# Kernel optimization log

Measured on AMD Instinct MI355X. Metric: run time of the kernel, lower is better.

## Reference

```python
import jax, jax.numpy as jnp
from jax import lax
import numpy as np

B, W, D = 32, 256, 512      # batch, input_window, d_model == feature_size
NHID = W // 2               # GAT hidden per head = 128
NHEADS = 4
ALPHA = 0.1                 # LeakyReLU slope (GAT default)
NEG = -1e9                  # masked-softmax fill


def conv1d(x, w, b):
    # x: [B, C, L], w: [O, I, K=3], 'same' padding, stride 1
    y = lax.conv_general_dilated(x, w, (1,), 'SAME', dimension_numbers=('NCH', 'OIH', 'NCH'))
    return y + b[None, :, None]


def gat_heads(h, adj, Wt, bb, ai, ai_b, aj, aj_b):
    # h: [B, N, F_in], adj: [B, N, N]; vectorized over NHEADS heads
    Wh = jnp.einsum('bnf,hof->bhno', h, Wt) + bb[None, :, None, :]   # [B,H,N,NHID]
    e1 = jnp.einsum('bhno,ho->bhn', Wh, ai) + ai_b[None, :, None]
    e2 = jnp.einsum('bhno,ho->bhn', Wh, aj) + aj_b[None, :, None]
    e = jax.nn.leaky_relu(e1[..., :, None] + e2[..., None, :], ALPHA)  # [B,H,N,N]
    att = jax.nn.softmax(jnp.where(adj[:, None] > 0, e, NEG), axis=-1)
    return jnp.einsum('bhnm,bhmo->bhno', att, Wh)


def gat_out(h, adj, Wt, bb, ai, ai_b, aj, aj_b):
    # h: [B, N, NHEADS*NHID] -> [B, N, W]
    Wh = h @ Wt.T + bb
    e1 = Wh @ ai + ai_b
    e2 = Wh @ aj + aj_b
    e = jax.nn.leaky_relu(e1[:, :, None] + e2[:, None, :], ALPHA)
    att = jax.nn.softmax(jnp.where(adj > 0, e, NEG), axis=-1)
    return jnp.einsum('bnm,bmo->bno', att, Wh)


def setup_inputs() -> dict:
    key = jax.random.key(0)
    ks = jax.random.split(key, 16)
    f32 = jnp.float32
    def xu(k, shape, fan_in):
        return jax.random.normal(k, shape, f32) * (1.414 / np.sqrt(fan_in))
    return {
        'x': jax.random.normal(ks[0], (B, W, D), f32),
        'qW': xu(ks[1], (D, D, 3), 3 * D), 'qb': jnp.zeros((D,), f32),
        'kW': xu(ks[2], (D, D, 3), 3 * D), 'kb': jnp.zeros((D,), f32),
        'vW': xu(ks[3], (D, D, 3), 3 * D), 'vb': jnp.zeros((D,), f32),
        'head_W': xu(ks[4], (NHEADS, NHID, W), W), 'head_b': jnp.zeros((NHEADS, NHID), f32),
        'head_ai': xu(ks[5], (NHEADS, NHID), NHID), 'head_ai_b': jnp.zeros((NHEADS,), f32),
        'head_aj': xu(ks[6], (NHEADS, NHID), NHID), 'head_aj_b': jnp.zeros((NHEADS,), f32),
        'out_W': xu(ks[7], (W, NHEADS * NHID), NHEADS * NHID), 'out_b': jnp.zeros((W,), f32),
        'out_ai': xu(ks[8], (W,), W), 'out_ai_b': jnp.zeros((), f32),
        'out_aj': xu(ks[9], (W,), W), 'out_aj_b': jnp.zeros((), f32),
        'proj_W': xu(ks[10], (D, D), D), 'proj_b': jnp.zeros((D,), f32),
    }


def reference(x, qW, qb, kW, kb, vW, vb,
              head_W, head_b, head_ai, head_ai_b, head_aj, head_aj_b,
              out_W, out_b, out_ai, out_ai_b, out_aj, out_aj_b,
              proj_W, proj_b):
    b, w, f = x.shape
    xt = jnp.transpose(x, (0, 2, 1))                 # [B, D, W]
    q = conv1d(xt, qW, qb)
    k = conv1d(xt, kW, kb)
    v = conv1d(xt, vW, vb)
    scale = 1.0 / jnp.sqrt(jnp.asarray(f, x.dtype))  # q.shape[-2] == d_model
    adj = jax.nn.sigmoid(jnp.einsum('bdw,bew->bde', q, k) * scale)  # [B, D, D]
    # GAT: nodes = feature dims (N=D), node features = window (W); dropout skipped (eval)
    hh = jax.nn.elu(gat_heads(v, adj, head_W, head_b, head_ai, head_ai_b, head_aj, head_aj_b))
    hcat = jnp.transpose(hh, (0, 2, 1, 3)).reshape(b, f, NHEADS * NHID)  # [B, D, 4*NHID]
    g = gat_out(hcat, adj, out_W, out_b, out_ai, out_ai_b, out_aj, out_aj_b)
    gat_y = jax.nn.log_softmax(jax.nn.elu(g), axis=2)  # [B, D, W]
    out = jnp.transpose(gat_y, (0, 2, 1)) @ proj_W.T + proj_b  # [B, W, D]
    return (out, adj)
```

## Files before the change

kernel.cpp:

```cpp
#include <hip/hip_runtime.h>
#include <math.h>

typedef unsigned short u16;
typedef __attribute__((ext_vector_type(8))) short short8;
typedef __attribute__((ext_vector_type(4))) float f32x4;

#define BB 32
#define WW 256
#define DD 512
#define NHEADS 4
#define NHID 128

__device__ __forceinline__ u16 f2bf(float f) {
  union { float f; unsigned int i; } x; x.f = f;
  unsigned int i = x.i;
  i += 0x7fffu + ((i >> 16) & 1u);
  return (u16)(i >> 16);
}
__device__ __forceinline__ float bf2f(u16 u) {
  union { float f; unsigned int i; } x; x.i = ((unsigned int)u) << 16; return x.f;
}

union BF8 { short8 v; u16 u[8]; };
union BF4 { ushort4 v; u16 u[4]; };

__global__ __launch_bounds__(256) void kprep_w(
    const float* __restrict__ qW, const float* __restrict__ kW, const float* __restrict__ vW,
    u16* __restrict__ Wt)
{
  int idx = blockIdx.x*256 + threadIdx.x;
  if (idx >= 3*DD*DD) return;
  int c = idx >> 18;
  int oi = idx & (DD*DD - 1);
  int i = oi & (DD-1);
  int o = oi >> 9;
  const float* W = (c==0) ? qW : (c==1) ? kW : vW;
  float w0 = W[oi*3+0], w1 = W[oi*3+1], w2 = W[oi*3+2];
  Wt[((size_t)(c*3+0)*DD + o)*DD + i] = f2bf(w0);
  Wt[((size_t)(c*3+1)*DD + o)*DD + i] = f2bf(w1);
  Wt[((size_t)(c*3+2)*DD + o)*DD + i] = f2bf(w2);
}

__global__ __launch_bounds__(256) void kcvt(const float* __restrict__ s, u16* __restrict__ d, int n) {
  int i = blockIdx.x*256 + threadIdx.x;
  if (i < n) d[i] = f2bf(s[i]);
}

__global__ __launch_bounds__(256) void kprep_a(
    const float* __restrict__ hW, const float* __restrict__ hai, const float* __restrict__ haib,
    const float* __restrict__ haj, const float* __restrict__ hajb,
    const float* __restrict__ hb,
    const float* __restrict__ oW, const float* __restrict__ oai, const float* __restrict__ oaib,
    const float* __restrict__ oaj, const float* __restrict__ oajb,
    const float* __restrict__ ob,
    float* __restrict__ ahat_i, float* __restrict__ ahat_j,
    float* __restrict__ oahat_i, float* __restrict__ oahat_j,
    float* __restrict__ cvec)
{
  int idx = blockIdx.x*256 + threadIdx.x;
  if (idx < 1024) {
    int h = idx >> 8, f = idx & 255;
    float s = 0.f;
    for (int o = 0; o < NHID; ++o) s += hW[((size_t)h*NHID + o)*WW + f] * hai[h*NHID + o];
    ahat_i[idx] = s;
  } else if (idx < 2048) {
    int t = idx - 1024; int h = t >> 8, f = t & 255;
    float s = 0.f;
    for (int o = 0; o < NHID; ++o) s += hW[((size_t)h*NHID + o)*WW + f] * haj[h*NHID + o];
    ahat_j[t] = s;
  } else if (idx < 2560) {
    int f = idx - 2048;
    float s = 0.f;
    for (int o = 0; o < WW; ++o) s += oW[(size_t)o*DD + f] * oai[o];
    oahat_i[f] = s;
  } else if (idx < 3072) {
    int f = idx - 2560;
    float s = 0.f;
    for (int o = 0; o < WW; ++o) s += oW[(size_t)o*DD + f] * oaj[o];
    oahat_j[f] = s;
  } else if (idx < 3082) {
    int t = idx - 3072;
    if (t < 4) {
      float s = 0.f;
      for (int o = 0; o < NHID; ++o) s += hb[t*NHID + o]*hai[t*NHID + o];
      cvec[t] = s + haib[t];
    } else if (t < 8) {
      int h = t - 4; float s = 0.f;
      for (int o = 0; o < NHID; ++o) s += hb[h*NHID + o]*haj[h*NHID + o];
      cvec[t] = s + hajb[h];
    } else if (t == 8) {
      float s = 0.f;
      for (int o = 0; o < WW; ++o) s += ob[o]*oai[o];
      cvec[8] = s + oaib[0];
    } else {
      float s = 0.f;
      for (int o = 0; o < WW; ++o) s += ob[o]*oaj[o];
      cvec[9] = s + oajb[0];
    }
  }
}

__global__ __launch_bounds__(256) void kprep_x(
    const float* __restrict__ x, int zb, int nrow8, u16* __restrict__ xpad)
{
  int idx8 = blockIdx.x*256 + threadIdx.x;
  if (idx8 >= nrow8) return;
  int i8 = idx8 & 63;
  int rowg = idx8 >> 6;
  int z = rowg / 258, r = rowg - z*258;
  int t = r - 1;
  BF8 o8;
  if (t >= 0 && t < WW) {
    const float* src = x + ((size_t)(zb+z)*WW + t)*DD + i8*8;
    float4 v0 = *reinterpret_cast<const float4*>(src);
    float4 v1 = *reinterpret_cast<const float4*>(src + 4);
    o8.u[0]=f2bf(v0.x); o8.u[1]=f2bf(v0.y); o8.u[2]=f2bf(v0.z); o8.u[3]=f2bf(v0.w);
    o8.u[4]=f2bf(v1.x); o8.u[5]=f2bf(v1.y); o8.u[6]=f2bf(v1.z); o8.u[7]=f2bf(v1.w);
  } else {
    #pragma unroll
    for (int j = 0; j < 8; ++j) o8.u[j] = 0;
  }
  *reinterpret_cast<short8*>(xpad + (size_t)rowg*DD + i8*8) = o8.v;
}

__global__ __launch_bounds__(256) void k1_mfma(
    const u16* __restrict__ xpad, const u16* __restrict__ Wt,
    const float* __restrict__ qb, const float* __restrict__ kb, const float* __restrict__ vb,
    u16* __restrict__ qbf, u16* __restrict__ kbf, u16* __restrict__ vbf)
{
  __shared__ u16 bt[2][130*64];
  const int tid = threadIdx.x;
  const int w  = tid >> 6;
  const int l  = tid & 63;
  const int ln = l & 15;
  const int kg = l >> 4;
  const int og = blockIdx.x * 64 + w * 16;
  const int t0 = blockIdx.y * 128;
  const int z  = blockIdx.z;

  const u16* A0 = Wt + (size_t)(og + ln)*DD + kg*8;
  const u16* Xb = xpad + ((size_t)z*258 + t0)*DD;

  f32x4 acc[3][8];
  #pragma unroll
  for (int c=0;c<3;++c)
    #pragma unroll
    for (int ts=0;ts<8;++ts) acc[c][ts] = (f32x4){0.f,0.f,0.f,0.f};

  short8 ArP[9], ArQ[9];
  short8 sg0, sg1, sg2, sg3, sg4;
  const int ccw = tid & 7;
  const int rs = tid >> 3;

#define K1_LOADX(i0v) do { \
    sg0 = *reinterpret_cast<const short8*>(Xb + (size_t)rs*DD + (i0v) + ccw*8); \
    sg1 = *reinterpret_cast<const short8*>(Xb + (size_t)(rs+32)*DD + (i0v) + ccw*8); \
    sg2 = *reinterpret_cast<const short8*>(Xb + (size_t)(rs+64)*DD + (i0v) + ccw*8); \
    sg3 = *reinterpret_cast<const short8*>(Xb + (size_t)(rs+96)*DD + (i0v) + ccw*8); \
    if (tid < 16) sg4 = *reinterpret_cast<const short8*>(Xb + (size_t)(rs+128)*DD + (i0v) + ccw*8); \
  } while(0)

#define K1_WRITEX(bufv) do { \
    *reinterpret_cast<short8*>(&bt[bufv][rs*64 + ((ccw^(rs&7))<<3)]) = sg0; \
    *reinterpret_cast<short8*>(&bt[bufv][(rs+32)*64 + ((ccw^((rs+32)&7))<<3)]) = sg1; \
    *reinterpret_cast<short8*>(&bt[bufv][(rs+64)*64 + ((ccw^((rs+64)&7))<<3)]) = sg2; \
    *reinterpret_cast<short8*>(&bt[bufv][(rs+96)*64 + ((ccw^((rs+96)&7))<<3)]) = sg3; \
    if (tid < 16) *reinterpret_cast<short8*>(&bt[bufv][(rs+128)*64 + ((ccw^((rs+128)&7))<<3)]) = sg4; \
  } while(0)

#define K1_LOADA(Abuf, i0v, khv) do { \
    _Pragma("unroll") \
    for (int c = 0; c < 3; ++c) { \
      _Pragma("unroll") \
      for (int tap = 0; tap < 3; ++tap) \
        Abuf[c*3+tap] = *reinterpret_cast<const short8*>(A0 + (size_t)(c*3+tap)*DD*DD + (i0v) + (khv)*32); \
    } \
  } while(0)

#define K1_MFMAS(Abuf, khv) do { \
    _Pragma("unroll") \
    for (int tap = 0; tap < 3; ++tap) { \
      _Pragma("unroll") \
      for (int ts = 0; ts < 8; ++ts) { \
        int row = ts*16 + ln + tap; \
        short8 bfr = *reinterpret_cast<const short8*>(&bt[cur][row*64 + ((((khv)*4+kg) ^ (row&7))<<3)]); \
        acc[0][ts] = __builtin_amdgcn_mfma_f32_16x16x32_bf16(Abuf[0*3+tap], bfr, acc[0][ts], 0,0,0); \
        acc[1][ts] = __builtin_amdgcn_mfma_f32_16x16x32_bf16(Abuf[1*3+tap], bfr, acc[1][ts], 0,0,0); \
        acc[2][ts] = __builtin_amdgcn_mfma_f32_16x16x32_bf16(Abuf[2*3+tap], bfr, acc[2][ts], 0,0,0); \
      } \
    } \
  } while(0)

  K1_LOADX(0);
  K1_LOADA(ArP, 0, 0);
  K1_WRITEX(0);
  __syncthreads();

  int cur = 0;
  #pragma unroll 1
  for (int p = 0; p < 8; ++p) {
    const int i0 = p*64;
    if (p < 7) K1_LOADX(i0 + 64);
    K1_LOADA(ArQ, i0, 1);
    K1_MFMAS(ArP, 0);
    const int i0n = (p < 7) ? i0 + 64 : 0;
    K1_LOADA(ArP, i0n, 0);
    K1_MFMAS(ArQ, 1);
    if (p < 7) {
      K1_WRITEX(cur ^ 1);
      __syncthreads();
      cur ^= 1;
    }
  }

#undef K1_LOADX
#undef K1_WRITEX
#undef K1_LOADA
#undef K1_MFMAS

  #pragma unroll
  for (int ts=0; ts<8; ++ts) {
    int tg = t0 + ts*16 + ln;
    #pragma unroll
    for (int r=0;r<4;++r) {
      int o = og + kg*4 + r;
      size_t oi = (size_t)(z*DD + o)*WW + tg;
      qbf[oi] = f2bf(acc[0][ts][r] + qb[o]);
      kbf[oi] = f2bf(acc[1][ts][r] + kb[o]);
      vbf[oi] = f2bf(acc[2][ts][r] + vb[o]);
    }
  }
}


__global__ __launch_bounds__(256) void k2_adj(
    const u16* __restrict__ qbf, const u16* __restrict__ kbf, int zb, float* __restrict__ adjo)
{
  __shared__ u16 bp[2][64*64];
  const int tid = threadIdx.x;
  const int w = tid >> 6, l = tid & 63, ln = l & 15, kg = l >> 4;
  const int d0 = blockIdx.x*64 + w*16;
  const int e0 = blockIdx.y*64;
  const int z  = blockIdx.z;
  const int sc = tid & 7, sr = tid >> 3;
  const int sp = sc ^ (sr & 7);
  const int sp2 = sc ^ ((sr+32) & 7);
  const u16* B0 = kbf + (size_t)(z*DD + e0)*WW;
  const u16* Asrc = qbf + (size_t)(z*DD + d0 + ln)*WW + kg*8;

  f32x4 acc[4];
  #pragma unroll
  for (int es=0;es<4;++es) acc[es] = (f32x4){0.f,0.f,0.f,0.f};
  short8 aP0, aP1, aQ0, aQ1, sg0, sg1;

  sg0 = *reinterpret_cast<const short8*>(B0 + (size_t)sr*WW + sc*8);
  sg1 = *reinterpret_cast<const short8*>(B0 + (size_t)(sr+32)*WW + sc*8);
  aP0 = *reinterpret_cast<const short8*>(Asrc);
  aP1 = *reinterpret_cast<const short8*>(Asrc + 32);
  *reinterpret_cast<short8*>(&bp[0][sr*64 + sp*8]) = sg0;
  *reinterpret_cast<short8*>(&bp[0][(sr+32)*64 + sp2*8]) = sg1;
  __syncthreads();

  int cur = 0;
  #pragma unroll 1
  for (int s = 0; s < 4; ++s) {
    const int fn = (s+1)*64;
    if (s < 3) {
      sg0 = *reinterpret_cast<const short8*>(B0 + (size_t)sr*WW + fn + sc*8);
      sg1 = *reinterpret_cast<const short8*>(B0 + (size_t)(sr+32)*WW + fn + sc*8);
      aQ0 = *reinterpret_cast<const short8*>(Asrc + fn);
      aQ1 = *reinterpret_cast<const short8*>(Asrc + fn + 32);
    }
    #pragma unroll
    for (int es = 0; es < 4; ++es) {
      int row = es*16 + ln;
      short8 b0 = *reinterpret_cast<const short8*>(&bp[cur][row*64 + ((kg ^ (row&7))<<3)]);
      acc[es] = __builtin_amdgcn_mfma_f32_16x16x32_bf16(aP0, b0, acc[es], 0,0,0);
      short8 b1 = *reinterpret_cast<const short8*>(&bp[cur][row*64 + (((4+kg) ^ (row&7))<<3)]);
      acc[es] = __builtin_amdgcn_mfma_f32_16x16x32_bf16(aP1, b1, acc[es], 0,0,0);
    }
    if (s < 3) {
      *reinterpret_cast<short8*>(&bp[cur^1][sr*64 + sp*8]) = sg0;
      *reinterpret_cast<short8*>(&bp[cur^1][(sr+32)*64 + sp2*8]) = sg1;
      __syncthreads();
      cur ^= 1;
      aP0 = aQ0; aP1 = aQ1;
    }
  }
  const float scale = 0.044194173824159216f;
  #pragma unroll
  for (int es=0; es<4; ++es)
    #pragma unroll
    for (int r=0; r<4; ++r) {
      float sig = 1.f/(1.f + expf(-acc[es][r]*scale));
      adjo[((size_t)(zb+z)*DD + d0 + kg*4 + r)*DD + e0 + es*16 + ln] = sig;
    }
}

__global__ __launch_bounds__(256) void k3_wh(
    const u16* __restrict__ vbf, const u16* __restrict__ hWbf, const float* __restrict__ hb,
    u16* __restrict__ Whtbf)
{
  __shared__ u16 bp[2][64*64];
  const int tid = threadIdx.x;
  const int w = tid >> 6, l = tid & 63, ln = l & 15, kg = l >> 4;
  const int n0 = blockIdx.x*64 + w*16;
  const int o0 = blockIdx.y*64;
  const int zh = blockIdx.z, z = zh >> 2, h = zh & 3;
  const int sc = tid & 7, sr = tid >> 3;
  const int sp = sc ^ (sr & 7);
  const int sp2 = sc ^ ((sr+32) & 7);
  const u16* B0 = hWbf + (size_t)(h*NHID + o0)*WW;
  const u16* Asrc = vbf + (size_t)(z*DD + n0 + ln)*WW + kg*8;

  f32x4 acc[4];
  #pragma unroll
  for (int os=0;os<4;++os) acc[os] = (f32x4){0.f,0.f,0.f,0.f};
  short8 aP0, aP1, aQ0, aQ1, sg0, sg1;

  sg0 = *reinterpret_cast<const short8*>(B0 + (size_t)sr*WW + sc*8);
  sg1 = *reinterpret_cast<const short8*>(B0 + (size_t)(sr+32)*WW + sc*8);
  aP0 = *reinterpret_cast<const short8*>(Asrc);
  aP1 = *reinterpret_cast<const short8*>(Asrc + 32);
  *reinterpret_cast<short8*>(&bp[0][sr*64 + sp*8]) = sg0;
  *reinterpret_cast<short8*>(&bp[0][(sr+32)*64 + sp2*8]) = sg1;
  __syncthreads();

  int cur = 0;
  #pragma unroll 1
  for (int s = 0; s < 4; ++s) {
    const int fn = (s+1)*64;
    if (s < 3) {
      sg0 = *reinterpret_cast<const short8*>(B0 + (size_t)sr*WW + fn + sc*8);
      sg1 = *reinterpret_cast<const short8*>(B0 + (size_t)(sr+32)*WW + fn + sc*8);
      aQ0 = *reinterpret_cast<const short8*>(Asrc + fn);
      aQ1 = *reinterpret_cast<const short8*>(Asrc + fn + 32);
    }
    #pragma unroll
    for (int os = 0; os < 4; ++os) {
      int row = os*16 + ln;
      short8 b0 = *reinterpret_cast<const short8*>(&bp[cur][row*64 + ((kg ^ (row&7))<<3)]);
      acc[os] = __builtin_amdgcn_mfma_f32_16x16x32_bf16(aP0, b0, acc[os], 0,0,0);
      short8 b1 = *reinterpret_cast<const short8*>(&bp[cur][row*64 + (((4+kg) ^ (row&7))<<3)]);
      acc[os] = __builtin_amdgcn_mfma_f32_16x16x32_bf16(aP1, b1, acc[os], 0,0,0);
    }
    if (s < 3) {
      *reinterpret_cast<short8*>(&bp[cur^1][sr*64 + sp*8]) = sg0;
      *reinterpret_cast<short8*>(&bp[cur^1][(sr+32)*64 + sp2*8]) = sg1;
      __syncthreads();
      cur ^= 1;
      aP0 = aQ0; aP1 = aQ1;
    }
  }
  #pragma unroll
  for (int os=0; os<4; ++os)
    #pragma unroll
    for (int r=0; r<4; ++r) {
      int o = o0 + os*16 + ln;
      int n = n0 + kg*4 + r;
      Whtbf[((size_t)zh*NHID + o)*DD + n] = f2bf(acc[os][r] + hb[h*NHID + o]);
    }
}

__global__ __launch_bounds__(256) void k4_eheads(
    const u16* __restrict__ vbf,
    const float* __restrict__ ahat_i, const float* __restrict__ ahat_j,
    const float* __restrict__ cvec,
    float* __restrict__ e1, float* __restrict__ e2)
{
  int row = blockIdx.x*4 + (threadIdx.x >> 6);
  int lane = threadIdx.x & 63;
  int zh = row >> 9, n = row & 511;
  int z = zh >> 2, h = zh & 3;
  BF4 v4; v4.v = *reinterpret_cast<const ushort4*>(vbf + ((size_t)(z*DD + n))*WW + lane*4);
  const float* aif = ahat_i + h*WW + lane*4;
  const float* ajf = ahat_j + h*WW + lane*4;
  float a1 = 0.f, a2 = 0.f;
  #pragma unroll
  for (int j = 0; j < 4; ++j) {
    float vf = bf2f(v4.u[j]);
    a1 += vf * aif[j];
    a2 += vf * ajf[j];
  }
  #pragma unroll
  for (int off = 32; off >= 1; off >>= 1) { a1 += __shfl_xor(a1, off); a2 += __shfl_xor(a2, off); }
  if (lane == 0) { e1[row] = a1 + cvec[h]; e2[row] = a2 + cvec[4+h]; }
}

__device__ __forceinline__ int attsw(int c, int row) {
  return c ^ ((c >> 3) & 7) ^ (row & 7);
}

__global__ __launch_bounds__(256) void k5_attn(
    const float* __restrict__ e1h, const float* __restrict__ e2h,
    const u16* __restrict__ Whtbf, u16* __restrict__ hcatbf)
{
  __shared__ u16 att[64*512];
  __shared__ float inv_lds[64];
  const int nb = blockIdx.x, zh = blockIdx.y;
  const int z = zh >> 2, h = zh & 3;
  const int n0 = nb*64;
  const int tid = threadIdx.x;

  const int r = tid >> 2, qd = tid & 3;
  const float e1n = e1h[(size_t)zh*DD + n0 + r];
  const float* e2r = e2h + (size_t)zh*DD + qd*128;
  float lmax = -1e30f;
  for (int j = 0; j < 128; ++j) {
    float e = e1n + e2r[j];
    e = (e > 0.f) ? e : 0.1f*e;
    lmax = fmaxf(lmax, e);
  }
  lmax = fmaxf(lmax, __shfl_xor(lmax, 1));
  lmax = fmaxf(lmax, __shfl_xor(lmax, 2));
  float lsum = 0.f;
  for (int jc = 0; jc < 16; ++jc) {
    BF8 pk;
    #pragma unroll
    for (int jj = 0; jj < 8; ++jj) {
      float e = e1n + e2r[jc*8 + jj];
      e = (e > 0.f) ? e : 0.1f*e;
      float p = expf(e - lmax);
      lsum += p;
      pk.u[jj] = f2bf(p);
    }
    int c = qd*16 + jc;
    *reinterpret_cast<short8*>(&att[r*512 + attsw(c, r)*8]) = pk.v;
  }
  lsum += __shfl_xor(lsum, 1);
  lsum += __shfl_xor(lsum, 2);
  if ((tid & 3) == 0) inv_lds[r] = 1.f / lsum;
  __syncthreads();

  const int w = tid >> 6, l = tid & 63, ln = l & 15, kg = l >> 4;
  const u16* B0 = Whtbf + ((size_t)zh*NHID + w*32 + ln)*DD + kg*8;
  f32x4 acc[4][2];
  #pragma unroll
  for (int ns=0; ns<4; ++ns) { acc[ns][0] = (f32x4){0,0,0,0}; acc[ns][1] = (f32x4){0,0,0,0}; }

  short8 Pb0,Pb1,Qb0,Qb1,Rb0,Rb1,Sb0,Sb1;
#define K5_LDB(R0,R1,kkv) do { int kc = ((kkv) < 16) ? (kkv) : 0; \
    R0 = *reinterpret_cast<const short8*>(B0 + (size_t)kc*32); \
    R1 = *reinterpret_cast<const short8*>(B0 + (size_t)16*DD + (size_t)kc*32); } while(0)
#define K5_MM(R0,R1,kkv) do { \
    _Pragma("unroll") \
    for (int ns = 0; ns < 4; ++ns) { \
      int row = ns*16 + ln; int c = (kkv)*4 + kg; \
      short8 af = *reinterpret_cast<const short8*>(&att[row*512 + attsw(c,row)*8]); \
      acc[ns][0] = __builtin_amdgcn_mfma_f32_16x16x32_bf16(af, R0, acc[ns][0], 0,0,0); \
      acc[ns][1] = __builtin_amdgcn_mfma_f32_16x16x32_bf16(af, R1, acc[ns][1], 0,0,0); \
    } } while(0)

  K5_LDB(Pb0,Pb1,0); K5_LDB(Qb0,Qb1,1); K5_LDB(Rb0,Rb1,2);
  #pragma unroll 1
  for (int kk = 0; kk < 16; kk += 4) {
    K5_LDB(Sb0,Sb1,kk+3); K5_MM(Pb0,Pb1,kk);
    K5_LDB(Pb0,Pb1,kk+4); K5_MM(Qb0,Qb1,kk+1);
    K5_LDB(Qb0,Qb1,kk+5); K5_MM(Rb0,Rb1,kk+2);
    K5_LDB(Rb0,Rb1,kk+6); K5_MM(Sb0,Sb1,kk+3);
  }
#undef K5_LDB
#undef K5_MM

  #pragma unroll
  for (int ns = 0; ns < 4; ++ns)
    #pragma unroll
    for (int rr = 0; rr < 4; ++rr) {
      int n = ns*16 + kg*4 + rr;
      float inv = inv_lds[n];
      #pragma unroll
      for (int j = 0; j < 2; ++j) {
        float s = acc[ns][j][rr] * inv;
        s = (s > 0.f) ? s : expm1f(s);
        hcatbf[((size_t)z*DD + n0 + n)*DD + h*NHID + w*32 + j*16 + ln] = f2bf(s);
      }
    }
}

__global__ __launch_bounds__(256) void k6_wh2(
    const u16* __restrict__ hcatbf, const u16* __restrict__ oWbf, const float* __restrict__ ob,
    u16* __restrict__ Wh2tbf)
{
  __shared__ u16 bp[2][64*64];
  const int tid = threadIdx.x;
  const int w = tid >> 6, l = tid & 63, ln = l & 15, kg = l >> 4;
  const int n0 = blockIdx.x*64 + w*16;
  const int o0 = blockIdx.y*64;
  const int z  = blockIdx.z;
  const int sc = tid & 7, sr = tid >> 3;
  const int sp = sc ^ (sr & 7);
  const int sp2 = sc ^ ((sr+32) & 7);
  const u16* B0 = oWbf + (size_t)o0*DD;
  const u16* Asrc = hcatbf + (size_t)(z*DD + n0 + ln)*DD + kg*8;

  f32x4 acc[4];
  #pragma unroll
  for (int os=0;os<4;++os) acc[os] = (f32x4){0.f,0.f,0.f,0.f};
  short8 aP0, aP1, aQ0, aQ1, sg0, sg1;

  sg0 = *reinterpret_cast<const short8*>(B0 + (size_t)sr*DD + sc*8);
  sg1 = *reinterpret_cast<const short8*>(B0 + (size_t)(sr+32)*DD + sc*8);
  aP0 = *reinterpret_cast<const short8*>(Asrc);
  aP1 = *reinterpret_cast<const short8*>(Asrc + 32);
  *reinterpret_cast<short8*>(&bp[0][sr*64 + sp*8]) = sg0;
  *reinterpret_cast<short8*>(&bp[0][(sr+32)*64 + sp2*8]) = sg1;
  __syncthreads();

  int cur = 0;
  #pragma unroll 1
  for (int s = 0; s < 8; ++s) {
    const int fn = (s+1)*64;
    if (s < 7) {
      sg0 = *reinterpret_cast<const short8*>(B0 + (size_t)sr*DD + fn + sc*8);
      sg1 = *reinterpret_cast<const short8*>(B0 + (size_t)(sr+32)*DD + fn + sc*8);
      aQ0 = *reinterpret_cast<const short8*>(Asrc + fn);
      aQ1 = *reinterpret_cast<const short8*>(Asrc + fn + 32);
    }
    #pragma unroll
    for (int os = 0; os < 4; ++os) {
      int row = os*16 + ln;
      short8 b0 = *reinterpret_cast<const short8*>(&bp[cur][row*64 + ((kg ^ (row&7))<<3)]);
      acc[os] = __builtin_amdgcn_mfma_f32_16x16x32_bf16(aP0, b0, acc[os], 0,0,0);
      short8 b1 = *reinterpret_cast<const short8*>(&bp[cur][row*64 + (((4+kg) ^ (row&7))<<3)]);
      acc[os] = __builtin_amdgcn_mfma_f32_16x16x32_bf16(aP1, b1, acc[os], 0,0,0);
    }
    if (s < 7) {
      *reinterpret_cast<short8*>(&bp[cur^1][sr*64 + sp*8]) = sg0;
      *reinterpret_cast<short8*>(&bp[cur^1][(sr+32)*64 + sp2*8]) = sg1;
      __syncthreads();
      cur ^= 1;
      aP0 = aQ0; aP1 = aQ1;
    }
  }
  #pragma unroll
  for (int os=0; os<4; ++os)
    #pragma unroll
    for (int r=0; r<4; ++r) {
      int o = o0 + os*16 + ln;
      int n = n0 + kg*4 + r;
      Wh2tbf[((size_t)z*WW + o)*DD + n] = f2bf(acc[os][r] + ob[o]);
    }
}

__global__ __launch_bounds__(256) void k7_eout(
    const u16* __restrict__ hcatbf,
    const float* __restrict__ oahat_i, const float* __restrict__ oahat_j,
    const float* __restrict__ cvec,
    float* __restrict__ e1, float* __restrict__ e2)
{
  int row = blockIdx.x*4 + (threadIdx.x >> 6);
  int lane = threadIdx.x & 63;
  BF8 v8; v8.v = *reinterpret_cast<const short8*>(hcatbf + (size_t)row*DD + lane*8);
  float a1 = 0.f, a2 = 0.f;
  #pragma unroll
  for (int j = 0; j < 8; ++j) {
    float vf = bf2f(v8.u[j]);
    a1 += vf * oahat_i[lane*8 + j];
    a2 += vf * oahat_j[lane*8 + j];
  }
  #pragma unroll
  for (int off = 32; off >= 1; off >>= 1) { a1 += __shfl_xor(a1, off); a2 += __shfl_xor(a2, off); }
  if (lane == 0) { e1[row] = a1 + cvec[8]; e2[row] = a2 + cvec[9]; }
}

__global__ __launch_bounds__(256) void k8_pv(
    const float* __restrict__ e1o, const float* __restrict__ e2o,
    const u16* __restrict__ Wh2tbf, float* __restrict__ g)
{
  __shared__ u16 att[64*512];
  __shared__ float inv_lds[64];
  const int nb = blockIdx.x, z = blockIdx.y, oh = blockIdx.z;
  const int n0 = nb*64;
  const int tid = threadIdx.x;

  const int r = tid >> 2, qd = tid & 3;
  const float e1n = e1o[(size_t)z*DD + n0 + r];
  const float* e2r = e2o + (size_t)z*DD + qd*128;
  float lmax = -1e30f;
  for (int j = 0; j < 128; ++j) {
    float e = e1n + e2r[j];
    e = (e > 0.f) ? e : 0.1f*e;
    lmax = fmaxf(lmax, e);
  }
  lmax = fmaxf(lmax, __shfl_xor(lmax, 1));
  lmax = fmaxf(lmax, __shfl_xor(lmax, 2));
  float lsum = 0.f;
  for (int jc = 0; jc < 16; ++jc) {
    BF8 pk;
    #pragma unroll
    for (int jj = 0; jj < 8; ++jj) {
      float e = e1n + e2r[jc*8 + jj];
      e = (e > 0.f) ? e : 0.1f*e;
      float p = expf(e - lmax);
      lsum += p;
      pk.u[jj] = f2bf(p);
    }
    int c = qd*16 + jc;
    *reinterpret_cast<short8*>(&att[r*512 + attsw(c, r)*8]) = pk.v;
  }
  lsum += __shfl_xor(lsum, 1);
  lsum += __shfl_xor(lsum, 2);
  if ((tid & 3) == 0) inv_lds[r] = 1.f / lsum;
  __syncthreads();

  const int w = tid >> 6, l = tid & 63, ln = l & 15, kg = l >> 4;
  const u16* B0 = Wh2tbf + ((size_t)z*WW + oh*128 + w*32 + ln)*DD + kg*8;
  f32x4 acc[4][2];
  #pragma unroll
  for (int ns=0; ns<4; ++ns) { acc[ns][0] = (f32x4){0,0,0,0}; acc[ns][1] = (f32x4){0,0,0,0}; }

  short8 Pb0,Pb1,Qb0,Qb1,Rb0,Rb1,Sb0,Sb1;
#define K8_LDB(R0,R1,kkv) do { int kc = ((kkv) < 16) ? (kkv) : 0; \
    R0 = *reinterpret_cast<const short8*>(B0 + (size_t)kc*32); \
    R1 = *reinterpret_cast<const short8*>(B0 + (size_t)16*DD + (size_t)kc*32); } while(0)
#define K8_MM(R0,R1,kkv) do { \
    _Pragma("unroll") \
    for (int ns = 0; ns < 4; ++ns) { \
      int row = ns*16 + ln; int c = (kkv)*4 + kg; \
      short8 af = *reinterpret_cast<const short8*>(&att[row*512 + attsw(c,row)*8]); \
      acc[ns][0] = __builtin_amdgcn_mfma_f32_16x16x32_bf16(af, R0, acc[ns][0], 0,0,0); \
      acc[ns][1] = __builtin_amdgcn_mfma_f32_16x16x32_bf16(af, R1, acc[ns][1], 0,0,0); \
    } } while(0)

  K8_LDB(Pb0,Pb1,0); K8_LDB(Qb0,Qb1,1); K8_LDB(Rb0,Rb1,2);
  #pragma unroll 1
  for (int kk = 0; kk < 16; kk += 4) {
    K8_LDB(Sb0,Sb1,kk+3); K8_MM(Pb0,Pb1,kk);
    K8_LDB(Pb0,Pb1,kk+4); K8_MM(Qb0,Qb1,kk+1);
    K8_LDB(Qb0,Qb1,kk+5); K8_MM(Rb0,Rb1,kk+2);
    K8_LDB(Rb0,Rb1,kk+6); K8_MM(Sb0,Sb1,kk+3);
  }
#undef K8_LDB
#undef K8_MM

  #pragma unroll
  for (int ns = 0; ns < 4; ++ns)
    #pragma unroll
    for (int rr = 0; rr < 4; ++rr) {
      int n = ns*16 + kg*4 + rr;
      float inv = inv_lds[n];
      #pragma unroll
      for (int j = 0; j < 2; ++j) {
        float val = acc[ns][j][rr] * inv;
        val = (val > 0.f) ? val : expm1f(val);
        g[((size_t)z*DD + n0 + n)*WW + oh*128 + w*32 + j*16 + ln] = val;
      }
    }
}

__global__ __launch_bounds__(256) void k8_lsm(
    const float* __restrict__ g, u16* __restrict__ gatybf)
{
  int row = blockIdx.x*4 + (threadIdx.x >> 6);
  int lane = threadIdx.x & 63;
  const float* gr = g + (size_t)row*WW;
  float v0 = gr[lane], v1 = gr[lane+64], v2 = gr[lane+128], v3 = gr[lane+192];
  float mx = fmaxf(fmaxf(v0,v1), fmaxf(v2,v3));
  #pragma unroll
  for (int off = 32; off >= 1; off >>= 1) mx = fmaxf(mx, __shfl_xor(mx, off));
  float sm = expf(v0-mx) + expf(v1-mx) + expf(v2-mx) + expf(v3-mx);
  #pragma unroll
  for (int off = 32; off >= 1; off >>= 1) sm += __shfl_xor(sm, off);
  float lg = mx + logf(sm);
  u16* go = gatybf + (size_t)row*WW;
  go[lane]     = f2bf(v0 - lg);
  go[lane+64]  = f2bf(v1 - lg);
  go[lane+128] = f2bf(v2 - lg);
  go[lane+192] = f2bf(v3 - lg);
}

__global__ __launch_bounds__(256) void k9_proj(
    const u16* __restrict__ gatybf, const u16* __restrict__ pWbf, const float* __restrict__ pb,
    int zb, float* __restrict__ out0)
{
  __shared__ u16 gt[64*40];
  const int t0 = blockIdx.x*64, d0 = blockIdx.y*64, z = blockIdx.z;
  const int tid = threadIdx.x;
  const int w = tid >> 6, l = tid & 63, ln = l & 15, kg = l >> 4;
  const int el = tid >> 3, t8 = tid & 7;
  f32x4 acc[4];
  #pragma unroll
  for (int os=0;os<4;++os) acc[os] = (f32x4){0.f,0.f,0.f,0.f};
  for (int e0 = 0; e0 < DD; e0 += 32) {
    __syncthreads();
    BF8 g8;
    g8.v = *reinterpret_cast<const short8*>(gatybf + ((size_t)z*DD + e0 + el)*WW + t0 + t8*8);
    #pragma unroll
    for (int j = 0; j < 8; ++j) gt[(t8*8 + j)*40 + el] = g8.u[j];
    __syncthreads();
    short8 a = *reinterpret_cast<const short8*>(&gt[(w*16 + ln)*40 + kg*8]);
    #pragma unroll
    for (int os = 0; os < 4; ++os) {
      short8 b = *reinterpret_cast<const short8*>(pWbf + (size_t)(d0 + os*16 + ln)*DD + e0 + kg*8);
      acc[os] = __builtin_amdgcn_mfma_f32_16x16x32_bf16(a, b, acc[os], 0,0,0);
    }
  }
  #pragma unroll
  for (int os=0; os<4; ++os)
    #pragma unroll
    for (int rr=0; rr<4; ++rr) {
      int t = t0 + w*16 + kg*4 + rr;
      int d = d0 + os*16 + ln;
      out0[((size_t)(zb+z)*WW + t)*DD + d] = acc[os][rr] + pb[d];
    }
}

extern "C" void kernel_launch(void* const* d_in, const int* in_sizes, int n_in,
                              void* d_out, int out_size, void* d_ws, size_t ws_size,
                              hipStream_t stream)
{
  const float* x   = (const float*)d_in[0];
  const float* qW  = (const float*)d_in[1];
  const float* qb  = (const float*)d_in[2];
  const float* kW  = (const float*)d_in[3];
  const float* kb  = (const float*)d_in[4];
  const float* vW  = (const float*)d_in[5];
  const float* vb  = (const float*)d_in[6];
  const float* hW  = (const float*)d_in[7];
  const float* hb  = (const float*)d_in[8];
  const float* hai = (const float*)d_in[9];
  const float* haib= (const float*)d_in[10];
  const float* haj = (const float*)d_in[11];
  const float* hajb= (const float*)d_in[12];
  const float* oW  = (const float*)d_in[13];
  const float* ob  = (const float*)d_in[14];
  const float* oai = (const float*)d_in[15];
  const float* oaib= (const float*)d_in[16];
  const float* oaj = (const float*)d_in[17];
  const float* oajb= (const float*)d_in[18];
  const float* pW  = (const float*)d_in[19];
  const float* pb  = (const float*)d_in[20];

  float* out0 = (float*)d_out;
  float* adjo = out0 + (size_t)BB*WW*DD;

  float* ws      = (float*)d_ws;
  u16*   Wt      = (u16*)(ws + 0);
  u16*   hWbf    = (u16*)(ws + 1179648);
  u16*   oWbf    = (u16*)(ws + 1245184);
  u16*   pWbf    = (u16*)(ws + 1310720);
  float* ahat_i  = ws + 1441792;
  float* ahat_j  = ws + 1442816;
  float* oahat_i = ws + 1443840;
  float* oahat_j = ws + 1444352;
  float* cvec    = ws + 1444864;
  float* e1h     = ws + 1444880;
  float* e2h     = ws + 1510416;
  float* e1o     = ws + 1575952;
  float* e2o     = ws + 1592336;
  const size_t X0 = 1608720;

  int CB = 4;
  {
    const int cand[3] = {32, 16, 8};
    for (int i = 0; i < 3; ++i) {
      size_t need = (X0 + (size_t)cand[i]*393728) * 4;
      if (need <= ws_size) { CB = cand[i]; break; }
    }
  }

  u16* xpad   = (u16*)(ws + X0);
  u16* vbf    = (u16*)(ws + X0 + (size_t)CB*66048);
  u16* qbf    = (u16*)(ws + X0 + (size_t)CB*131584);
  u16* kbf    = (u16*)(ws + X0 + (size_t)CB*197120);
  u16* Whtbf  = (u16*)(ws + X0 + (size_t)CB*262656);
  u16*   hcatbf = (u16*)(ws + X0);
  float* g      = (float*)(ws + X0);
  u16*   gatybf = (u16*)(ws + X0 + (size_t)CB*131584);
  u16*   Wh2tbf = (u16*)(ws + X0 + (size_t)CB*197120);

  kprep_w<<<dim3((3*DD*DD + 255)/256), 256, 0, stream>>>(qW, kW, vW, Wt);
  kcvt<<<dim3((NHEADS*NHID*WW + 255)/256), 256, 0, stream>>>(hW, hWbf, NHEADS*NHID*WW);
  kcvt<<<dim3((WW*DD + 255)/256), 256, 0, stream>>>(oW, oWbf, WW*DD);
  kcvt<<<dim3((DD*DD + 255)/256), 256, 0, stream>>>(pW, pWbf, DD*DD);
  kprep_a<<<dim3(13), 256, 0, stream>>>(hW, hai, haib, haj, hajb, hb,
                                        oW, oai, oaib, oaj, oajb, ob,
                                        ahat_i, ahat_j, oahat_i, oahat_j, cvec);

  for (int zb = 0; zb < BB; zb += CB) {
    int nrow8 = CB*258*64;
    kprep_x  <<<dim3((nrow8 + 255)/256), 256, 0, stream>>>(x, zb, nrow8, xpad);
    k1_mfma  <<<dim3(DD/64, WW/128, CB), 256, 0, stream>>>(xpad, Wt, qb, kb, vb, qbf, kbf, vbf);
    k2_adj   <<<dim3(DD/64, DD/64, CB), 256, 0, stream>>>(qbf, kbf, zb, adjo);
    k3_wh    <<<dim3(DD/64, NHID/64, CB*NHEADS), 256, 0, stream>>>(vbf, hWbf, hb, Whtbf);
    k4_eheads<<<dim3(CB*NHEADS*DD/4), 256, 0, stream>>>(vbf, ahat_i, ahat_j, cvec, e1h, e2h);
    k5_attn  <<<dim3(DD/64, CB*NHEADS), 256, 0, stream>>>(e1h, e2h, Whtbf, hcatbf);
    k6_wh2   <<<dim3(DD/64, WW/64, CB), 256, 0, stream>>>(hcatbf, oWbf, ob, Wh2tbf);
    k7_eout  <<<dim3(CB*DD/4), 256, 0, stream>>>(hcatbf, oahat_i, oahat_j, cvec, e1o, e2o);
    k8_pv    <<<dim3(DD/64, CB, 2), 256, 0, stream>>>(e1o, e2o, Wh2tbf, g);
    k8_lsm   <<<dim3(CB*128), 256, 0, stream>>>(g, gatybf);
    k9_proj  <<<dim3(WW/64, DD/64, CB), 256, 0, stream>>>(gatybf, pWbf, pb, zb, out0);
  }
}
```

Measured before the change: 324.1 us.

## Factor leaky-ReLU softmax exponentials into per-column precomputed terms and remap blocks per XCD

Removes the per-row max-reduction pass and the per-element expf in the two GAT softmax kernels. Because e = leaky(e1+e2) splits into two exponential branches, exp(e2-M2) and exp(0.1*(e2-M2)) are precomputed once per head in a new kexp2 kernel. Each element then costs one compare and one multiply by a per-row scale. The attention kernels are also flattened to 1D grids, with a block index remap that groups blocks of the same head or batch onto the same XCD for L2 locality. The cost is an extra small kernel launch, and the row normaliser is no longer the true row max, which could hurt numerical stability for large logit ranges.

```diff
diff --git a/kernel.cpp b/kernel.cpp
--- a/kernel.cpp
+++ b/kernel.cpp
@@ -23,6 +23,7 @@
 
 union BF8 { short8 v; u16 u[8]; };
 union BF4 { ushort4 v; u16 u[4]; };
+union F8 { float4 v4[2]; float f[8]; };
 
 __global__ __launch_bounds__(256) void kprep_w(
     const float* __restrict__ qW, const float* __restrict__ kW, const float* __restrict__ vW,
@@ -123,6 +124,26 @@
   *reinterpret_cast<short8*>(xpad + (size_t)rowg*DD + i8*8) = o8.v;
 }
 
+__global__ __launch_bounds__(256) void kexp2(
+    const float* __restrict__ e2, float* __restrict__ M2,
+    float* __restrict__ E2p, float* __restrict__ E2n)
+{
+  __shared__ float s4[4];
+  const int zh = blockIdx.x, tid = threadIdx.x;
+  float v0 = e2[(size_t)zh*DD + tid], v1 = e2[(size_t)zh*DD + 256 + tid];
+  float m = fmaxf(v0, v1);
+  #pragma unroll
+  for (int off=32; off>=1; off>>=1) m = fmaxf(m, __shfl_xor(m, off));
+  if ((tid & 63) == 0) s4[tid >> 6] = m;
+  __syncthreads();
+  m = fmaxf(fmaxf(s4[0], s4[1]), fmaxf(s4[2], s4[3]));
+  if (tid == 0) M2[zh] = m;
+  E2p[(size_t)zh*DD + tid]       = expf(v0 - m);
+  E2p[(size_t)zh*DD + 256 + tid] = expf(v1 - m);
+  E2n[(size_t)zh*DD + tid]       = expf(0.1f*(v0 - m));
+  E2n[(size_t)zh*DD + 256 + tid] = expf(0.1f*(v1 - m));
+}
+
 __global__ __launch_bounds__(256) void k1_mfma(
     const u16* __restrict__ xpad, const u16* __restrict__ Wt,
     const float* __restrict__ qb, const float* __restrict__ kb, const float* __restrict__ vb,
@@ -232,7 +253,6 @@
   }
 }
 
-
 __global__ __launch_bounds__(256) void k2_adj(
     const u16* __restrict__ qbf, const u16* __restrict__ kbf, int zb, float* __restrict__ adjo)
 {
@@ -393,34 +413,45 @@
 
 __global__ __launch_bounds__(256) void k5_attn(
     const float* __restrict__ e1h, const float* __restrict__ e2h,
-    const u16* __restrict__ Whtbf, u16* __restrict__ hcatbf)
+    const float* __restrict__ M2h, const float* __restrict__ E2p, const float* __restrict__ E2n,
+    const u16* __restrict__ Whtbf, u16* __restrict__ hcatbf, int nzh)
 {
   __shared__ u16 att[64*512];
   __shared__ float inv_lds[64];
-  const int nb = blockIdx.x, zh = blockIdx.y;
+  const int orig = blockIdx.x;
+  const int xcd = orig & 7;
+  const int k = orig >> 3;
+  const int nb = k & 7;
+  const int zh = xcd * (nzh >> 3) + (k >> 3);
   const int z = zh >> 2, h = zh & 3;
   const int n0 = nb*64;
   const int tid = threadIdx.x;
 
   const int r = tid >> 2, qd = tid & 3;
   const float e1n = e1h[(size_t)zh*DD + n0 + r];
+  const float M2 = M2h[zh];
+  const float s = e1n + M2;
+  const float mx = (s > 0.f) ? s : 0.1f*s;
+  const float Ap = expf(s - mx);
+  const float An = expf(0.1f*s - mx);
+  const float thr = -e1n;
   const float* e2r = e2h + (size_t)zh*DD + qd*128;
-  float lmax = -1e30f;
-  for (int j = 0; j < 128; ++j) {
-    float e = e1n + e2r[j];
-    e = (e > 0.f) ? e : 0.1f*e;
-    lmax = fmaxf(lmax, e);
-  }
-  lmax = fmaxf(lmax, __shfl_xor(lmax, 1));
-  lmax = fmaxf(lmax, __shfl_xor(lmax, 2));
+  const float* Epr = E2p + (size_t)zh*DD + qd*128;
+  const float* Enr = E2n + (size_t)zh*DD + qd*128;
   float lsum = 0.f;
   for (int jc = 0; jc < 16; ++jc) {
+    int j0 = jc*8;
+    F8 e2x, epx, enx;
+    e2x.v4[0] = *reinterpret_cast<const float4*>(e2r + j0);
+    e2x.v4[1] = *reinterpret_cast<const float4*>(e2r + j0 + 4);
+    epx.v4[0] = *reinterpret_cast<const float4*>(Epr + j0);
+    epx.v4[1] = *reinterpret_cast<const float4*>(Epr + j0 + 4);
+    enx.v4[0] = *reinterpret_cast<const float4*>(Enr + j0);
+    enx.v4[1] = *reinterpret_cast<const float4*>(Enr + j0 + 4);
     BF8 pk;
     #pragma unroll
     for (int jj = 0; jj < 8; ++jj) {
-      float e = e1n + e2r[jc*8 + jj];
-      e = (e > 0.f) ? e : 0.1f*e;
-      float p = expf(e - lmax);
+      float p = (e2x.f[jj] > thr) ? Ap * epx.f[jj] : An * enx.f[jj];
       lsum += p;
       pk.u[jj] = f2bf(p);
     }
@@ -470,9 +501,9 @@
       float inv = inv_lds[n];
       #pragma unroll
       for (int j = 0; j < 2; ++j) {
-        float s = acc[ns][j][rr] * inv;
-        s = (s > 0.f) ? s : expm1f(s);
-        hcatbf[((size_t)z*DD + n0 + n)*DD + h*NHID + w*32 + j*16 + ln] = f2bf(s);
+        float sv = acc[ns][j][rr] * inv;
+        sv = (sv > 0.f) ? sv : expm1f(sv);
+        hcatbf[((size_t)z*DD + n0 + n)*DD + h*NHID + w*32 + j*16 + ln] = f2bf(sv);
       }
     }
 }
@@ -565,33 +596,54 @@
 
 __global__ __launch_bounds__(256) void k8_pv(
     const float* __restrict__ e1o, const float* __restrict__ e2o,
-    const u16* __restrict__ Wh2tbf, float* __restrict__ g)
+    const float* __restrict__ M2o, const float* __restrict__ E2p, const float* __restrict__ E2n,
+    const u16* __restrict__ Wh2tbf, float* __restrict__ g, int CBv)
 {
   __shared__ u16 att[64*512];
   __shared__ float inv_lds[64];
-  const int nb = blockIdx.x, z = blockIdx.y, oh = blockIdx.z;
+  const int orig = blockIdx.x;
+  int nb, z, oh;
+  if (CBv >= 8) {
+    int xcd = orig & 7;
+    int k = orig >> 3;
+    nb = k & 7;
+    int rest = k >> 3;
+    oh = rest & 1;
+    z = xcd * (CBv >> 3) + (rest >> 1);
+  } else {
+    nb = orig & 7;
+    int k = orig >> 3;
+    z = k >> 1;
+    oh = k & 1;
+  }
   const int n0 = nb*64;
   const int tid = threadIdx.x;
 
   const int r = tid >> 2, qd = tid & 3;
   const float e1n = e1o[(size_t)z*DD + n0 + r];
+  const float M2 = M2o[z];
+  const float s = e1n + M2;
+  const float mx = (s > 0.f) ? s : 0.1f*s;
+  const float Ap = expf(s - mx);
+  const float An = expf(0.1f*s - mx);
+  const float thr = -e1n;
   const float* e2r = e2o + (size_t)z*DD + qd*128;
-  float lmax = -1e30f;
-  for (int j = 0; j < 128; ++j) {
-    float e = e1n + e2r[j];
-    e = (e > 0.f) ? e : 0.1f*e;
-    lmax = fmaxf(lmax, e);
-  }
-  lmax = fmaxf(lmax, __shfl_xor(lmax, 1));
-  lmax = fmaxf(lmax, __shfl_xor(lmax, 2));
+  const float* Epr = E2p + (size_t)z*DD + qd*128;
+  const float* Enr = E2n + (size_t)z*DD + qd*128;
   float lsum = 0.f;
   for (int jc = 0; jc < 16; ++jc) {
+    int j0 = jc*8;
+    F8 e2x, epx, enx;
+    e2x.v4[0] = *reinterpret_cast<const float4*>(e2r + j0);
+    e2x.v4[1] = *reinterpret_cast<const float4*>(e2r + j0 + 4);
+    epx.v4[0] = *reinterpret_cast<const float4*>(Epr + j0);
+    epx.v4[1] = *reinterpret_cast<const float4*>(Epr + j0 + 4);
+    enx.v4[0] = *reinterpret_cast<const float4*>(Enr + j0);
+    enx.v4[1] = *reinterpret_cast<const float4*>(Enr + j0 + 4);
     BF8 pk;
     #pragma unroll
     for (int jj = 0; jj < 8; ++jj) {
-      float e = e1n + e2r[jc*8 + jj];
-      e = (e > 0.f) ? e : 0.1f*e;
-      float p = expf(e - lmax);
+      float p = (e2x.f[jj] > thr) ? Ap * epx.f[jj] : An * enx.f[jj];
       lsum += p;
       pk.u[jj] = f2bf(p);
     }
@@ -748,7 +800,13 @@
   float* e2h     = ws + 1510416;
   float* e1o     = ws + 1575952;
   float* e2o     = ws + 1592336;
-  const size_t X0 = 1608720;
+  float* M2h     = ws + 1608720;
+  float* E2hp    = ws + 1608848;
+  float* E2hn    = ws + 1674384;
+  float* M2o     = ws + 1739920;
+  float* E2op    = ws + 1739952;
+  float* E2on    = ws + 1756336;
+  const size_t X0 = 1772720;
 
   int CB = 4;
   {
@@ -784,10 +842,12 @@
     k2_adj   <<<dim3(DD/64, DD/64, CB), 256, 0, stream>>>(qbf, kbf, zb, adjo);
     k3_wh    <<<dim3(DD/64, NHID/64, CB*NHEADS), 256, 0, stream>>>(vbf, hWbf, hb, Whtbf);
     k4_eheads<<<dim3(CB*NHEADS*DD/4), 256, 0, stream>>>(vbf, ahat_i, ahat_j, cvec, e1h, e2h);
-    k5_attn  <<<dim3(DD/64, CB*NHEADS), 256, 0, stream>>>(e1h, e2h, Whtbf, hcatbf);
+    kexp2    <<<dim3(CB*NHEADS), 256, 0, stream>>>(e2h, M2h, E2hp, E2hn);
+    k5_attn  <<<dim3(32*CB), 256, 0, stream>>>(e1h, e2h, M2h, E2hp, E2hn, Whtbf, hcatbf, CB*NHEADS);
     k6_wh2   <<<dim3(DD/64, WW/64, CB), 256, 0, stream>>>(hcatbf, oWbf, ob, Wh2tbf);
     k7_eout  <<<dim3(CB*DD/4), 256, 0, stream>>>(hcatbf, oahat_i, oahat_j, cvec, e1o, e2o);
-    k8_pv    <<<dim3(DD/64, CB, 2), 256, 0, stream>>>(e1o, e2o, Wh2tbf, g);
+    kexp2    <<<dim3(CB), 256, 0, stream>>>(e2o, M2o, E2op, E2on);
+    k8_pv    <<<dim3(16*CB), 256, 0, stream>>>(e1o, e2o, M2o, E2op, E2on, Wh2tbf, g, CB);
     k8_lsm   <<<dim3(CB*128), 256, 0, stream>>>(g, gatybf);
     k9_proj  <<<dim3(WW/64, DD/64, CB), 256, 0, stream>>>(gatybf, pWbf, pb, zb, out0);
   }
```

After: 332.0 us. 1.02x slower.
